# Kernel optimization log

Measured on AMD Instinct MI355X. Metric: run time of the kernel, lower is better.

Reference implementation:

```python
import jax, jax.numpy as jnp
import numpy as np

N_NODES = 100000
N_EDGES = 600000
N_GRAPHS = 512


def _glorot(key, shape):
    fan_in, fan_out = shape
    lim = np.sqrt(6.0 / (fan_in + fan_out)).astype(np.float32)
    return jax.random.uniform(key, shape, jnp.float32, -lim, lim)


def setup_inputs() -> dict:
    key = jax.random.key(0)
    ks = jax.random.split(key, 12)
    x = jax.random.normal(ks[0], (N_NODES, 3), jnp.float32)
    edge_index = jax.random.randint(ks[1], (2, N_EDGES), 0, N_NODES, jnp.int64)
    batch = jnp.sort(jax.random.randint(ks[2], (N_NODES,), 0, N_GRAPHS, jnp.int64))
    return {
        "x": x,
        "edge_index": edge_index,
        "batch": batch,
        "W1": _glorot(ks[3], (3, 128)),   "b1": jnp.zeros((128,), jnp.float32),
        "W2": _glorot(ks[4], (128, 128)), "b2": jnp.zeros((128,), jnp.float32),
        "W3": _glorot(ks[5], (128, 64)),  "b3": jnp.zeros((64,), jnp.float32),
        "Wl": _glorot(ks[6], (64, 1)),    "bl": jnp.zeros((1,), jnp.float32),
    }


def _gcn_conv(h, W, b, src, dst, deg_inv_sqrt):
    # linear transform, then normalized gather-scatter aggregation (self-loops
    # already included in src/dst and deg_inv_sqrt).
    h = h @ W                                            # [N, F_out]
    norm = deg_inv_sqrt[src] * deg_inv_sqrt[dst]         # [E+N]
    msg = h[src] * norm[:, None]                         # [E+N, F_out]
    out = jax.ops.segment_sum(msg, dst, num_segments=N_NODES)
    return out + b


def reference(x, edge_index, batch, W1, b1, W2, b2, W3, b3, Wl, bl):
    # add self-loops (GCNConv default add_self_loops=True)
    loop = jnp.arange(N_NODES, dtype=edge_index.dtype)
    src = jnp.concatenate([edge_index[0], loop])
    dst = jnp.concatenate([edge_index[1], loop])
    # symmetric normalization deg^{-1/2} (in-degree at target, edge weight 1)
    deg = jax.ops.segment_sum(jnp.ones_like(dst, jnp.float32), dst,
                              num_segments=N_NODES)
    deg_inv_sqrt = jnp.where(deg > 0, jax.lax.rsqrt(jnp.maximum(deg, 1.0)), 0.0)

    h = jax.nn.relu(_gcn_conv(x, W1, b1, src, dst, deg_inv_sqrt))
    h = jax.nn.relu(_gcn_conv(h, W2, b2, src, dst, deg_inv_sqrt))
    h = jax.nn.relu(_gcn_conv(h, W3, b3, src, dst, deg_inv_sqrt))

    # global mean pool over graphs
    sums = jax.ops.segment_sum(h, batch, num_segments=N_GRAPHS)    # [G, 64]
    counts = jax.ops.segment_sum(jnp.ones((N_NODES,), jnp.float32), batch,
                                 num_segments=N_GRAPHS)
    pooled = sums / jnp.maximum(counts, 1.0)[:, None]

    return pooled @ Wl + bl                                        # [G, 1]
```

## Files before the change

### kernel.cpp

```cpp
#include <hip/hip_runtime.h>

#define N_NODES 100000
#define N_EDGES 600000
#define N_GRAPHS 512

typedef __attribute__((ext_vector_type(8))) short short8;
typedef __attribute__((ext_vector_type(4))) float floatx4;
typedef __attribute__((ext_vector_type(2))) float floatx2;

__device__ __forceinline__ unsigned short f2bf(float f) {
    unsigned int u = __float_as_uint(f);
    u += 0x7FFFu + ((u >> 16) & 1u);
    return (unsigned short)(u >> 16);
}
__device__ __forceinline__ short8 pack8(const float* a) {
    short8 r;
    #pragma unroll
    for (int j = 0; j < 8; ++j) r[j] = (short)f2bf(a[j]);
    return r;
}

__device__ __forceinline__ uint2 pack_fp8x8(const float* v) {
    uint2 r;
    unsigned int a = 0;
    a = __builtin_amdgcn_cvt_pk_fp8_f32(v[0], v[1], a, 0);
    a = __builtin_amdgcn_cvt_pk_fp8_f32(v[2], v[3], a, 1);
    unsigned int b = 0;
    b = __builtin_amdgcn_cvt_pk_fp8_f32(v[4], v[5], b, 0);
    b = __builtin_amdgcn_cvt_pk_fp8_f32(v[6], v[7], b, 1);
    r.x = a; r.y = b;
    return r;
}
__device__ __forceinline__ unsigned char f2fp8(float v) {
    return (unsigned char)(__builtin_amdgcn_cvt_pk_fp8_f32(v, v, 0u, 0) & 0xFFu);
}
__device__ __forceinline__ void fma8_fp8(float* a, uint2 v, float n) {
    floatx2 p;
    p = __builtin_amdgcn_cvt_pk_f32_fp8(v.x, 0); a[0] = fmaf(p[0], n, a[0]); a[1] = fmaf(p[1], n, a[1]);
    p = __builtin_amdgcn_cvt_pk_f32_fp8(v.x, 1); a[2] = fmaf(p[0], n, a[2]); a[3] = fmaf(p[1], n, a[3]);
    p = __builtin_amdgcn_cvt_pk_f32_fp8(v.y, 0); a[4] = fmaf(p[0], n, a[4]); a[5] = fmaf(p[1], n, a[5]);
    p = __builtin_amdgcn_cvt_pk_f32_fp8(v.y, 1); a[6] = fmaf(p[0], n, a[6]); a[7] = fmaf(p[1], n, a[7]);
}
__device__ __forceinline__ void init8_fp8(float* a, uint2 v, float s) {
    floatx2 p;
    p = __builtin_amdgcn_cvt_pk_f32_fp8(v.x, 0); a[0] = p[0] * s; a[1] = p[1] * s;
    p = __builtin_amdgcn_cvt_pk_f32_fp8(v.x, 1); a[2] = p[0] * s; a[3] = p[1] * s;
    p = __builtin_amdgcn_cvt_pk_f32_fp8(v.y, 0); a[4] = p[0] * s; a[5] = p[1] * s;
    p = __builtin_amdgcn_cvt_pk_f32_fp8(v.y, 1); a[6] = p[0] * s; a[7] = p[1] * s;
}

__global__ void k_hist(const int* __restrict__ dst, int* cnt) {
    int e = blockIdx.x * 256 + threadIdx.x;
    if (e < N_EDGES) atomicAdd(&cnt[dst[e]], 1);
}

__global__ void k_scan1(const int* __restrict__ cnt, int* __restrict__ part) {
    __shared__ int s[256];
    int t = threadIdx.x;
    int i = blockIdx.x * 256 + t;
    int v = (i < N_NODES) ? cnt[i] : 0;
    s[t] = v; __syncthreads();
    for (int off = 128; off > 0; off >>= 1) {
        if (t < off) s[t] += s[t + off];
        __syncthreads();
    }
    if (t == 0) part[blockIdx.x] = s[0];
}

__global__ void k_scan3(const int* __restrict__ cnt, const int* __restrict__ part,
                        int* __restrict__ row_ptr, int* __restrict__ cursor,
                        float* __restrict__ dis) {
    __shared__ int s[256];
    __shared__ int pbaseS;
    int t = threadIdx.x;
    int psum = 0;
    for (int k = t; k < blockIdx.x; k += 256) psum += part[k];
    s[t] = psum; __syncthreads();
    for (int off = 128; off > 0; off >>= 1) {
        if (t < off) s[t] += s[t + off];
        __syncthreads();
    }
    if (t == 0) pbaseS = s[0];
    __syncthreads();
    int pbase = pbaseS;
    __syncthreads();
    int i = blockIdx.x * 256 + t;
    int v = (i < N_NODES) ? cnt[i] : 0;
    s[t] = v; __syncthreads();
    for (int off = 1; off < 256; off <<= 1) {
        int u = (t >= off) ? s[t - off] : 0;
        __syncthreads();
        s[t] += u;
        __syncthreads();
    }
    int ex = s[t] - v + pbase;
    if (i < N_NODES) {
        row_ptr[i] = ex; cursor[i] = ex;
        dis[i] = 1.0f / sqrtf((float)(v + 1));
    }
    if (blockIdx.x == 0 && t == 0) row_ptr[N_NODES] = N_EDGES;
}

__global__ void k_scatter(const int* __restrict__ src, const int* __restrict__ dst,
                          const float* __restrict__ dis, int* __restrict__ cursor,
                          int* __restrict__ csr_src, float* __restrict__ csr_norm) {
    int e = blockIdx.x * 256 + threadIdx.x;
    if (e >= N_EDGES) return;
    int s = src[e], d = dst[e];
    int pos = atomicAdd(&cursor[d], 1);
    csr_src[pos] = s;
    csr_norm[pos] = dis[s] * dis[d];
}

__device__ __forceinline__ void pack_one(const float* __restrict__ W, unsigned short* __restrict__ out,
                                         int idx, int N) {
    int lane = idx & 63;
    int ks = (idx >> 6) & 3;
    int ct = idx >> 8;
    int n = ct * 16 + (lane & 15);
    int kbase = ks * 32 + (lane >> 4) * 8;
    #pragma unroll
    for (int j = 0; j < 8; ++j)
        out[(size_t)idx * 8 + j] = f2bf(W[(size_t)(kbase + j) * N + n]);
}

#define NB1 6250
__global__ __launch_bounds__(256) void k_node1(const float* __restrict__ x,
                                               const float* __restrict__ dis,
                                               const int* __restrict__ row_ptr,
                                               const int* __restrict__ csr_src,
                                               const float* __restrict__ csr_norm,
                                               const float* __restrict__ W1,
                                               const float* __restrict__ b1,
                                               unsigned char* __restrict__ out,
                                               const float* __restrict__ W2,
                                               const float* __restrict__ W3,
                                               unsigned short* __restrict__ Wp2,
                                               unsigned short* __restrict__ Wp3) {
    int tid = threadIdx.x;
    if (blockIdx.x >= NB1) {
        int idx = (blockIdx.x - NB1) * 256 + tid;
        if (idx < 2048) pack_one(W2, Wp2, idx, 128);
        else if (idx < 3072) pack_one(W3, Wp3, idx - 2048, 64);
        return;
    }
    __shared__ float Ws[384];
    __shared__ float bs[128];
    for (int i = tid; i < 384; i += 256) Ws[i] = W1[i];
    if (tid < 128) bs[tid] = b1[tid];
    __syncthreads();
    int gw = (blockIdx.x * 256 + tid) >> 6;
    int lane = tid & 63;
    int sub = lane >> 4, l16 = lane & 15;
    int node = gw * 4 + sub;
    int beg = row_ptr[node], end = row_ptr[node + 1];
    float p0 = 0.f, p1 = 0.f, p2 = 0.f;
    for (int e = beg + l16; e < end; e += 16) {
        int s = csr_src[e];
        float n = csr_norm[e];
        p0 = fmaf(x[s * 3 + 0], n, p0);
        p1 = fmaf(x[s * 3 + 1], n, p1);
        p2 = fmaf(x[s * 3 + 2], n, p2);
    }
    #pragma unroll
    for (int m = 8; m > 0; m >>= 1) {
        p0 += __shfl_xor(p0, m, 64);
        p1 += __shfl_xor(p1, m, 64);
        p2 += __shfl_xor(p2, m, 64);
    }
    float d = dis[node], s2 = d * d;
    float a0 = fmaf(x[node * 3 + 0], s2, p0);
    float a1 = fmaf(x[node * 3 + 1], s2, p1);
    float a2 = fmaf(x[node * 3 + 2], s2, p2);
    int f = l16 * 8;
    float v[8];
    #pragma unroll
    for (int j = 0; j < 8; ++j)
        v[j] = fmaxf(bs[f + j] + a0 * Ws[f + j] + a1 * Ws[128 + f + j] + a2 * Ws[256 + f + j], 0.f);
    *(uint2*)(out + (size_t)node * 128 + f) = pack_fp8x8(v);
}

__global__ __launch_bounds__(256) void k_layer23(const unsigned char* __restrict__ h1,
                                                 const float* __restrict__ dis,
                                                 const int* __restrict__ row_ptr,
                                                 const int* __restrict__ csr_src,
                                                 const float* __restrict__ csr_norm,
                                                 const unsigned short* __restrict__ Wp2,
                                                 const float* __restrict__ b2,
                                                 const unsigned short* __restrict__ Wp3,
                                                 unsigned char* __restrict__ Q2f8) {
    __shared__ unsigned short Asb[16][136];
    __shared__ unsigned short Hsb[16][136];
    int tid = threadIdx.x;
    int wave = tid >> 6, lane = tid & 63;
    int quad = lane >> 4, m16 = lane & 15;
    int base = blockIdx.x * 16;

    {
        int sub = lane >> 4, l16 = lane & 15;
        int r = wave * 4 + sub;
        int node = base + r;
        int beg = row_ptr[node], end = row_ptr[node + 1];
        int idx[8]; float nn[8];
        #pragma unroll
        for (int u = 0; u < 8; ++u) {
            int ee = beg + u; int cl = ee < end ? ee : end - 1;
            idx[u] = csr_src[cl]; nn[u] = ee < end ? csr_norm[cl] : 0.0f;
        }
        float d = dis[node];
        uint2 self = *(const uint2*)(h1 + (size_t)node * 128 + l16 * 8);
        uint2 g[8];
        #pragma unroll
        for (int u = 0; u < 8; ++u)
            g[u] = *(const uint2*)(h1 + (size_t)idx[u] * 128 + l16 * 8);
        float a[8];
        init8_fp8(a, self, d * d);
        #pragma unroll
        for (int u = 0; u < 8; ++u) fma8_fp8(a, g[u], nn[u]);
        for (int e = beg + 8; e < end; e += 8) {
            int idx2[8]; float nn2[8];
            #pragma unroll
            for (int u = 0; u < 8; ++u) {
                int ee = e + u; int cl = ee < end ? ee : end - 1;
                idx2[u] = csr_src[cl]; nn2[u] = ee < end ? csr_norm[cl] : 0.0f;
            }
            uint2 g2[8];
            #pragma unroll
            for (int u = 0; u < 8; ++u)
                g2[u] = *(const uint2*)(h1 + (size_t)idx2[u] * 128 + l16 * 8);
            #pragma unroll
            for (int u = 0; u < 8; ++u) fma8_fp8(a, g2[u], nn2[u]);
        }
        *(short8*)(&Asb[r][l16 * 8]) = pack8(a);
    }
    __syncthreads();

    {
        short8 af[4];
        #pragma unroll
        for (int ks = 0; ks < 4; ++ks)
            af[ks] = *(const short8*)(&Asb[m16][ks * 32 + quad * 8]);
        floatx4 acc[2];
        acc[0] = (floatx4){0.f, 0.f, 0.f, 0.f};
        acc[1] = (floatx4){0.f, 0.f, 0.f, 0.f};
        #pragma unroll
        for (int c = 0; c < 2; ++c) {
            int gct = wave * 2 + c;
            #pragma unroll
            for (int ks = 0; ks < 4; ++ks) {
                short8 bf = *(const short8*)(Wp2 + ((size_t)(gct * 4 + ks) * 64 + lane) * 8);
                acc[c] = __builtin_amdgcn_mfma_f32_16x16x32_bf16(af[ks], bf, acc[c], 0, 0, 0);
            }
        }
        #pragma unroll
        for (int c = 0; c < 2; ++c) {
            int col = (wave * 2 + c) * 16 + m16;
            float bv = b2[col];
            #pragma unroll
            for (int r = 0; r < 4; ++r) {
                int row = quad * 4 + r;
                Hsb[row][col] = f2bf(fmaxf(acc[c][r] + bv, 0.0f));
            }
        }
    }
    __syncthreads();

    {
        short8 hf[4];
        #pragma unroll
        for (int ks = 0; ks < 4; ++ks)
            hf[ks] = *(const short8*)(&Hsb[m16][ks * 32 + quad * 8]);
        floatx4 acc3 = (floatx4){0.f, 0.f, 0.f, 0.f};
        #pragma unroll
        for (int ks = 0; ks < 4; ++ks) {
            short8 bf = *(const short8*)(Wp3 + ((size_t)(wave * 4 + ks) * 64 + lane) * 8);
            acc3 = __builtin_amdgcn_mfma_f32_16x16x32_bf16(hf[ks], bf, acc3, 0, 0, 0);
        }
        int col = wave * 16 + m16;
        #pragma unroll
        for (int r = 0; r < 4; ++r) {
            long row = base + quad * 4 + r;
            Q2f8[row * 64 + col] = f2fp8(acc3[r]);
        }
    }
}

__global__ __launch_bounds__(256) void k_agg64_dot(const unsigned char* __restrict__ h,
                                                   const float* __restrict__ dis,
                                                   const int* __restrict__ row_ptr,
                                                   const int* __restrict__ csr_src,
                                                   const float* __restrict__ csr_norm,
                                                   const float* __restrict__ bias,
                                                   const float* __restrict__ Wl,
                                                   float* __restrict__ s_out) {
    int gw = (blockIdx.x * 256 + threadIdx.x) >> 6;
    int lane = threadIdx.x & 63;
    int sub = lane >> 3, l8 = lane & 7;
    int node = gw * 8 + sub;
    int beg = row_ptr[node], end = row_ptr[node + 1];
    int idx[8]; float nn[8];
    #pragma unroll
    for (int u = 0; u < 8; ++u) {
        int ee = beg + u; int cl = ee < end ? ee : end - 1;
        idx[u] = csr_src[cl]; nn[u] = ee < end ? csr_norm[cl] : 0.0f;
    }
    float d = dis[node];
    uint2 self = *(const uint2*)(h + (size_t)node * 64 + l8 * 8);
    uint2 g[8];
    #pragma unroll
    for (int u = 0; u < 8; ++u)
        g[u] = *(const uint2*)(h + (size_t)idx[u] * 64 + l8 * 8);
    float a[8];
    init8_fp8(a, self, d * d);
    #pragma unroll
    for (int u = 0; u < 8; ++u) fma8_fp8(a, g[u], nn[u]);
    for (int e = beg + 8; e < end; e += 8) {
        int idx2[8]; float nn2[8];
        #pragma unroll
        for (int u = 0; u < 8; ++u) {
            int ee = e + u; int cl = ee < end ? ee : end - 1;
            idx2[u] = csr_src[cl]; nn2[u] = ee < end ? csr_norm[cl] : 0.0f;
        }
        uint2 g2[8];
        #pragma unroll
        for (int u = 0; u < 8; ++u)
            g2[u] = *(const uint2*)(h + (size_t)idx2[u] * 64 + l8 * 8);
        #pragma unroll
        for (int u = 0; u < 8; ++u) fma8_fp8(a, g2[u], nn2[u]);
    }
    int f = l8 * 8;
    float v = 0.f;
    #pragma unroll
    for (int j = 0; j < 8; ++j)
        v = fmaf(fmaxf(a[j] + bias[f + j], 0.f), Wl[f + j], v);
    #pragma unroll
    for (int m = 4; m > 0; m >>= 1) v += __shfl_xor(v, m, 64);
    if (l8 == 0) s_out[node] = v;
}

__global__ __launch_bounds__(256) void k_pool2(const float* __restrict__ s,
                                               const int* __restrict__ batch,
                                               const float* __restrict__ bl,
                                               float* __restrict__ out) {
    int g = blockIdx.x;
    int tid = threadIdx.x;
    int lo = 0, hi = N_NODES;
    while (lo < hi) { int m = (lo + hi) >> 1; if (batch[m] < g) lo = m + 1; else hi = m; }
    int lo2 = lo, hi2 = N_NODES;
    while (lo2 < hi2) { int m = (lo2 + hi2) >> 1; if (batch[m] < g + 1) lo2 = m + 1; else hi2 = m; }
    float acc = 0.0f;
    for (int n = lo + tid; n < lo2; n += 256) acc += s[n];
    __shared__ float sm[256];
    sm[tid] = acc; __syncthreads();
    for (int off = 128; off > 0; off >>= 1) {
        if (tid < off) sm[tid] += sm[tid + off];
        __syncthreads();
    }
    if (tid == 0) out[g] = sm[0] / fmaxf((float)(lo2 - lo), 1.0f) + bl[0];
}

extern "C" void kernel_launch(void* const* d_in, const int* in_sizes, int n_in,
                              void* d_out, int out_size, void* d_ws, size_t ws_size,
                              hipStream_t stream) {
    const float* x     = (const float*)d_in[0];
    const int*   ei    = (const int*)d_in[1];
    const int*   batch = (const int*)d_in[2];
    const float* W1 = (const float*)d_in[3];
    const float* b1 = (const float*)d_in[4];
    const float* W2 = (const float*)d_in[5];
    const float* b2 = (const float*)d_in[6];
    const float* W3 = (const float*)d_in[7];
    const float* b3 = (const float*)d_in[8];
    const float* Wl = (const float*)d_in[9];
    const float* bl = (const float*)d_in[10];
    float* out = (float*)d_out;

    const int* e_src = ei;
    const int* e_dst = ei + N_EDGES;

    char* ws = (char*)d_ws;
    size_t off = 0;
    auto alloc = [&](size_t bytes) -> char* {
        char* p = ws + off;
        off = (off + bytes + 255) & ~(size_t)255;
        return p;
    };
    int*   cnt      = (int*)  alloc((size_t)N_NODES * 4);
    float* dis      = (float*)alloc((size_t)N_NODES * 4);
    int*   row_ptr  = (int*)  alloc((size_t)(N_NODES + 1) * 4);
    int*   cursor   = (int*)  alloc((size_t)N_NODES * 4);
    int*   part     = (int*)  alloc(1024 * 4);
    int*   csr_src  = (int*)  alloc((size_t)N_EDGES * 4);
    float* csr_norm = (float*)alloc((size_t)N_EDGES * 4);
    float* nscal    = (float*)alloc((size_t)N_NODES * 4);
    unsigned char*  P1f8 = (unsigned char*) alloc((size_t)N_NODES * 128);
    unsigned char*  Q2f8 = (unsigned char*) alloc((size_t)N_NODES * 64);
    unsigned short* Wp2  = (unsigned short*)alloc((size_t)128 * 128 * 2);
    unsigned short* Wp3  = (unsigned short*)alloc((size_t)128 * 64 * 2);

    const int NB_N = (N_NODES + 255) / 256;
    const int NB_E = (N_EDGES + 255) / 256;

    hipMemsetAsync(cnt, 0, (size_t)N_NODES * 4, stream);
    k_hist<<<NB_E, 256, 0, stream>>>(e_dst, cnt);
    k_scan1<<<NB_N, 256, 0, stream>>>(cnt, part);
    k_scan3<<<NB_N, 256, 0, stream>>>(cnt, part, row_ptr, cursor, dis);
    k_scatter<<<NB_E, 256, 0, stream>>>(e_src, e_dst, dis, cursor, csr_src, csr_norm);

    k_node1<<<NB1 + 12, 256, 0, stream>>>(x, dis, row_ptr, csr_src, csr_norm,
                                          W1, b1, P1f8, W2, W3, Wp2, Wp3);

    k_layer23<<<N_NODES / 16, 256, 0, stream>>>(P1f8, dis, row_ptr, csr_src, csr_norm,
                                                Wp2, b2, Wp3, Q2f8);

    k_agg64_dot<<<N_NODES / 8 / 4, 256, 0, stream>>>(Q2f8, dis, row_ptr, csr_src, csr_norm,
                                                     b3, Wl, nscal);

    k_pool2<<<N_GRAPHS, 256, 0, stream>>>(nscal, batch, bl, out);
}
```

Measured before the change: 209.0 us.

## Widen gather loads to 16 bytes and double nodes per block in aggregation kernels

The gather-aggregate loops in k_layer23 and k_agg64_dot now read 16 fp8 features per lane as uint4 instead of 8 as uint2, so each wave covers twice as many nodes. k_layer23 processes 32 nodes per block and splits the 32x128 and 32x64 MFMA GEMMs across waves by row tile and column group. The wider loads are meant to cut load instruction count and raise memory-level parallelism on the random neighbor gathers. In exchange, each lane holds more registers (16 accumulators and eight uint4 gathers), which may reduce occupancy, and there are half as many blocks.

```diff
diff --git a/kernel.cpp b/kernel.cpp
--- a/kernel.cpp
+++ b/kernel.cpp
@@ -34,19 +34,23 @@
 __device__ __forceinline__ unsigned char f2fp8(float v) {
     return (unsigned char)(__builtin_amdgcn_cvt_pk_fp8_f32(v, v, 0u, 0) & 0xFFu);
 }
-__device__ __forceinline__ void fma8_fp8(float* a, uint2 v, float n) {
+__device__ __forceinline__ void fma4_fp8(float* a, unsigned int w, float n) {
     floatx2 p;
-    p = __builtin_amdgcn_cvt_pk_f32_fp8(v.x, 0); a[0] = fmaf(p[0], n, a[0]); a[1] = fmaf(p[1], n, a[1]);
-    p = __builtin_amdgcn_cvt_pk_f32_fp8(v.x, 1); a[2] = fmaf(p[0], n, a[2]); a[3] = fmaf(p[1], n, a[3]);
-    p = __builtin_amdgcn_cvt_pk_f32_fp8(v.y, 0); a[4] = fmaf(p[0], n, a[4]); a[5] = fmaf(p[1], n, a[5]);
-    p = __builtin_amdgcn_cvt_pk_f32_fp8(v.y, 1); a[6] = fmaf(p[0], n, a[6]); a[7] = fmaf(p[1], n, a[7]);
-}
-__device__ __forceinline__ void init8_fp8(float* a, uint2 v, float s) {
+    p = __builtin_amdgcn_cvt_pk_f32_fp8(w, 0); a[0] = fmaf(p[0], n, a[0]); a[1] = fmaf(p[1], n, a[1]);
+    p = __builtin_amdgcn_cvt_pk_f32_fp8(w, 1); a[2] = fmaf(p[0], n, a[2]); a[3] = fmaf(p[1], n, a[3]);
+}
+__device__ __forceinline__ void init4_fp8(float* a, unsigned int w, float s) {
     floatx2 p;
-    p = __builtin_amdgcn_cvt_pk_f32_fp8(v.x, 0); a[0] = p[0] * s; a[1] = p[1] * s;
-    p = __builtin_amdgcn_cvt_pk_f32_fp8(v.x, 1); a[2] = p[0] * s; a[3] = p[1] * s;
-    p = __builtin_amdgcn_cvt_pk_f32_fp8(v.y, 0); a[4] = p[0] * s; a[5] = p[1] * s;
-    p = __builtin_amdgcn_cvt_pk_f32_fp8(v.y, 1); a[6] = p[0] * s; a[7] = p[1] * s;
+    p = __builtin_amdgcn_cvt_pk_f32_fp8(w, 0); a[0] = p[0] * s; a[1] = p[1] * s;
+    p = __builtin_amdgcn_cvt_pk_f32_fp8(w, 1); a[2] = p[0] * s; a[3] = p[1] * s;
+}
+__device__ __forceinline__ void fma16_fp8(float* a, uint4 v, float n) {
+    fma4_fp8(a +  0, v.x, n); fma4_fp8(a +  4, v.y, n);
+    fma4_fp8(a +  8, v.z, n); fma4_fp8(a + 12, v.w, n);
+}
+__device__ __forceinline__ void init16_fp8(float* a, uint4 v, float s) {
+    init4_fp8(a +  0, v.x, s); init4_fp8(a +  4, v.y, s);
+    init4_fp8(a +  8, v.z, s); init4_fp8(a + 12, v.w, s);
 }
 
 __global__ void k_hist(const int* __restrict__ dst, int* cnt) {
@@ -189,16 +193,16 @@
                                                  const float* __restrict__ b2,
                                                  const unsigned short* __restrict__ Wp3,
                                                  unsigned char* __restrict__ Q2f8) {
-    __shared__ unsigned short Asb[16][136];
-    __shared__ unsigned short Hsb[16][136];
+    __shared__ unsigned short Asb[32][136];
+    __shared__ unsigned short Hsb[32][136];
     int tid = threadIdx.x;
     int wave = tid >> 6, lane = tid & 63;
     int quad = lane >> 4, m16 = lane & 15;
-    int base = blockIdx.x * 16;
+    int base = blockIdx.x * 32;
 
     {
-        int sub = lane >> 4, l16 = lane & 15;
-        int r = wave * 4 + sub;
+        int sub = lane >> 3, l8 = lane & 7;
+        int r = wave * 8 + sub;
         int node = base + r;
         int beg = row_ptr[node], end = row_ptr[node + 1];
         int idx[8]; float nn[8];
@@ -208,15 +212,15 @@
             idx[u] = csr_src[cl]; nn[u] = ee < end ? csr_norm[cl] : 0.0f;
         }
         float d = dis[node];
-        uint2 self = *(const uint2*)(h1 + (size_t)node * 128 + l16 * 8);
-        uint2 g[8];
+        uint4 self = *(const uint4*)(h1 + (size_t)node * 128 + l8 * 16);
+        uint4 g[8];
         #pragma unroll
         for (int u = 0; u < 8; ++u)
-            g[u] = *(const uint2*)(h1 + (size_t)idx[u] * 128 + l16 * 8);
-        float a[8];
-        init8_fp8(a, self, d * d);
-        #pragma unroll
-        for (int u = 0; u < 8; ++u) fma8_fp8(a, g[u], nn[u]);
+            g[u] = *(const uint4*)(h1 + (size_t)idx[u] * 128 + l8 * 16);
+        float a[16];
+        init16_fp8(a, self, d * d);
+        #pragma unroll
+        for (int u = 0; u < 8; ++u) fma16_fp8(a, g[u], nn[u]);
         for (int e = beg + 8; e < end; e += 8) {
             int idx2[8]; float nn2[8];
             #pragma unroll
@@ -224,63 +228,76 @@
                 int ee = e + u; int cl = ee < end ? ee : end - 1;
                 idx2[u] = csr_src[cl]; nn2[u] = ee < end ? csr_norm[cl] : 0.0f;
             }
-            uint2 g2[8];
+            uint4 g2[8];
             #pragma unroll
             for (int u = 0; u < 8; ++u)
-                g2[u] = *(const uint2*)(h1 + (size_t)idx2[u] * 128 + l16 * 8);
-            #pragma unroll
-            for (int u = 0; u < 8; ++u) fma8_fp8(a, g2[u], nn2[u]);
-        }
-        *(short8*)(&Asb[r][l16 * 8]) = pack8(a);
+                g2[u] = *(const uint4*)(h1 + (size_t)idx2[u] * 128 + l8 * 16);
+            #pragma unroll
+            for (int u = 0; u < 8; ++u) fma16_fp8(a, g2[u], nn2[u]);
+        }
+        *(short8*)(&Asb[r][l8 * 16])     = pack8(a);
+        *(short8*)(&Asb[r][l8 * 16 + 8]) = pack8(a + 8);
     }
     __syncthreads();
 
+    int mt = wave & 1;
+    int ch = wave >> 1;
     {
         short8 af[4];
         #pragma unroll
         for (int ks = 0; ks < 4; ++ks)
-            af[ks] = *(const short8*)(&Asb[m16][ks * 32 + quad * 8]);
-        floatx4 acc[2];
-        acc[0] = (floatx4){0.f, 0.f, 0.f, 0.f};
-        acc[1] = (floatx4){0.f, 0.f, 0.f, 0.f};
-        #pragma unroll
-        for (int c = 0; c < 2; ++c) {
-            int gct = wave * 2 + c;
+            af[ks] = *(const short8*)(&Asb[mt * 16 + m16][ks * 32 + quad * 8]);
+        floatx4 acc[4];
+        #pragma unroll
+        for (int ct = 0; ct < 4; ++ct) acc[ct] = (floatx4){0.f, 0.f, 0.f, 0.f};
+        #pragma unroll
+        for (int ct = 0; ct < 4; ++ct) {
+            int gct = ch * 4 + ct;
             #pragma unroll
             for (int ks = 0; ks < 4; ++ks) {
                 short8 bf = *(const short8*)(Wp2 + ((size_t)(gct * 4 + ks) * 64 + lane) * 8);
-                acc[c] = __builtin_amdgcn_mfma_f32_16x16x32_bf16(af[ks], bf, acc[c], 0, 0, 0);
+                acc[ct] = __builtin_amdgcn_mfma_f32_16x16x32_bf16(af[ks], bf, acc[ct], 0, 0, 0);
             }
         }
         #pragma unroll
-        for (int c = 0; c < 2; ++c) {
-            int col = (wave * 2 + c) * 16 + m16;
+        for (int ct = 0; ct < 4; ++ct) {
+            int col = (ch * 4 + ct) * 16 + m16;
             float bv = b2[col];
             #pragma unroll
             for (int r = 0; r < 4; ++r) {
-                int row = quad * 4 + r;
-                Hsb[row][col] = f2bf(fmaxf(acc[c][r] + bv, 0.0f));
+                int row = mt * 16 + quad * 4 + r;
+                Hsb[row][col] = f2bf(fmaxf(acc[ct][r] + bv, 0.0f));
             }
         }
     }
     __syncthreads();
 
     {
+        int cp = wave >> 1;
         short8 hf[4];
         #pragma unroll
         for (int ks = 0; ks < 4; ++ks)
-            hf[ks] = *(const short8*)(&Hsb[m16][ks * 32 + quad * 8]);
-        floatx4 acc3 = (floatx4){0.f, 0.f, 0.f, 0.f};
-        #pragma unroll
-        for (int ks = 0; ks < 4; ++ks) {
-            short8 bf = *(const short8*)(Wp3 + ((size_t)(wave * 4 + ks) * 64 + lane) * 8);
-            acc3 = __builtin_amdgcn_mfma_f32_16x16x32_bf16(hf[ks], bf, acc3, 0, 0, 0);
-        }
-        int col = wave * 16 + m16;
-        #pragma unroll
-        for (int r = 0; r < 4; ++r) {
-            long row = base + quad * 4 + r;
-            Q2f8[row * 64 + col] = f2fp8(acc3[r]);
+            hf[ks] = *(const short8*)(&Hsb[mt * 16 + m16][ks * 32 + quad * 8]);
+        floatx4 acc3[2];
+        acc3[0] = (floatx4){0.f, 0.f, 0.f, 0.f};
+        acc3[1] = (floatx4){0.f, 0.f, 0.f, 0.f};
+        #pragma unroll
+        for (int ct = 0; ct < 2; ++ct) {
+            int gct = cp * 2 + ct;
+            #pragma unroll
+            for (int ks = 0; ks < 4; ++ks) {
+                short8 bf = *(const short8*)(Wp3 + ((size_t)(gct * 4 + ks) * 64 + lane) * 8);
+                acc3[ct] = __builtin_amdgcn_mfma_f32_16x16x32_bf16(hf[ks], bf, acc3[ct], 0, 0, 0);
+            }
+        }
+        #pragma unroll
+        for (int ct = 0; ct < 2; ++ct) {
+            int col = (cp * 2 + ct) * 16 + m16;
+            #pragma unroll
+            for (int r = 0; r < 4; ++r) {
+                long row = base + mt * 16 + quad * 4 + r;
+                Q2f8[row * 64 + col] = f2fp8(acc3[ct][r]);
+            }
         }
     }
 }
@@ -294,9 +311,10 @@
                                                    const float* __restrict__ Wl,
                                                    float* __restrict__ s_out) {
     int gw = (blockIdx.x * 256 + threadIdx.x) >> 6;
+    if (gw >= N_NODES / 16) return;
     int lane = threadIdx.x & 63;
-    int sub = lane >> 3, l8 = lane & 7;
-    int node = gw * 8 + sub;
+    int sub = lane >> 2, l4 = lane & 3;
+    int node = gw * 16 + sub;
     int beg = row_ptr[node], end = row_ptr[node + 1];
     int idx[8]; float nn[8];
     #pragma unroll
@@ -305,15 +323,15 @@
         idx[u] = csr_src[cl]; nn[u] = ee < end ? csr_norm[cl] : 0.0f;
     }
     float d = dis[node];
-    uint2 self = *(const uint2*)(h + (size_t)node * 64 + l8 * 8);
-    uint2 g[8];
+    uint4 self = *(const uint4*)(h + (size_t)node * 64 + l4 * 16);
+    uint4 g[8];
     #pragma unroll
     for (int u = 0; u < 8; ++u)
-        g[u] = *(const uint2*)(h + (size_t)idx[u] * 64 + l8 * 8);
-    float a[8];
-    init8_fp8(a, self, d * d);
-    #pragma unroll
-    for (int u = 0; u < 8; ++u) fma8_fp8(a, g[u], nn[u]);
+        g[u] = *(const uint4*)(h + (size_t)idx[u] * 64 + l4 * 16);
+    float a[16];
+    init16_fp8(a, self, d * d);
+    #pragma unroll
+    for (int u = 0; u < 8; ++u) fma16_fp8(a, g[u], nn[u]);
     for (int e = beg + 8; e < end; e += 8) {
         int idx2[8]; float nn2[8];
         #pragma unroll
@@ -321,21 +339,21 @@
             int ee = e + u; int cl = ee < end ? ee : end - 1;
             idx2[u] = csr_src[cl]; nn2[u] = ee < end ? csr_norm[cl] : 0.0f;
         }
-        uint2 g2[8];
+        uint4 g2[8];
         #pragma unroll
         for (int u = 0; u < 8; ++u)
-            g2[u] = *(const uint2*)(h + (size_t)idx2[u] * 64 + l8 * 8);
-        #pragma unroll
-        for (int u = 0; u < 8; ++u) fma8_fp8(a, g2[u], nn2[u]);
-    }
-    int f = l8 * 8;
+            g2[u] = *(const uint4*)(h + (size_t)idx2[u] * 64 + l4 * 16);
+        #pragma unroll
+        for (int u = 0; u < 8; ++u) fma16_fp8(a, g2[u], nn2[u]);
+    }
+    int f = l4 * 16;
     float v = 0.f;
     #pragma unroll
-    for (int j = 0; j < 8; ++j)
+    for (int j = 0; j < 16; ++j)
         v = fmaf(fmaxf(a[j] + bias[f + j], 0.f), Wl[f + j], v);
-    #pragma unroll
-    for (int m = 4; m > 0; m >>= 1) v += __shfl_xor(v, m, 64);
-    if (l8 == 0) s_out[node] = v;
+    v += __shfl_xor(v, 1, 64);
+    v += __shfl_xor(v, 2, 64);
+    if (l4 == 0) s_out[node] = v;
 }
 
 __global__ __launch_bounds__(256) void k_pool2(const float* __restrict__ s,
@@ -410,11 +428,11 @@
     k_node1<<<NB1 + 12, 256, 0, stream>>>(x, dis, row_ptr, csr_src, csr_norm,
                                           W1, b1, P1f8, W2, W3, Wp2, Wp3);
 
-    k_layer23<<<N_NODES / 16, 256, 0, stream>>>(P1f8, dis, row_ptr, csr_src, csr_norm,
+    k_layer23<<<N_NODES / 32, 256, 0, stream>>>(P1f8, dis, row_ptr, csr_src, csr_norm,
                                                 Wp2, b2, Wp3, Q2f8);
 
-    k_agg64_dot<<<N_NODES / 8 / 4, 256, 0, stream>>>(Q2f8, dis, row_ptr, csr_src, csr_norm,
-                                                     b3, Wl, nscal);
+    k_agg64_dot<<<(N_NODES / 16 + 3) / 4, 256, 0, stream>>>(Q2f8, dis, row_ptr, csr_src, csr_norm,
+                                                            b3, Wl, nscal);
 
     k_pool2<<<N_GRAPHS, 256, 0, stream>>>(nscal, batch, bl, out);
 }
```

After: 204.0 us, median of 3. -2.4%, faster.
